# Kernel optimization log

Measured on AMD Instinct MI355X. Metric: run time of the kernel, lower is better.

## Reference

```python
import jax, jax.numpy as jnp
import numpy as np

B, EMB, H, G, F, CH, O, OC, KT = 4096, 256, 256, 8, 96, 16, 5, 10, 5
BN_EPS = 1e-3


def _grouped_linear(x, w):
    # x: [B, I], w: [G, I//G, O//G] -> [B, O]
    b = x.shape[0]
    g, ig, og = w.shape
    xg = x.reshape(b, g, ig)
    return jnp.einsum('bgi,gio->bgo', xg, w).reshape(b, g * og)


def _gru_cell(x, h, k, rk, bias):
    # keras GRUCell, reset_after=True; gate order z, r, h; bias: [2, 3H]
    xs = x @ k + bias[0]
    hs = h @ rk + bias[1]
    xz, xr, xh = jnp.split(xs, 3, axis=-1)
    hz, hr, hh = jnp.split(hs, 3, axis=-1)
    z = jax.nn.sigmoid(xz + hz)
    r = jax.nn.sigmoid(xr + hr)
    cand = jnp.tanh(xh + r * hh)
    return z * h + (1.0 - z) * cand


def setup_inputs() -> dict:
    key = jax.random.key(0)
    ks = jax.random.split(key, 20)
    w = lambda i, shape: (jax.random.normal(ks[i], shape, dtype=jnp.float32) * 0.05)
    inp = {
        'emb': jax.random.normal(ks[0], (B, EMB), dtype=jnp.float32),
        'c0': jax.random.normal(ks[1], (B, 1, F, CH), dtype=jnp.float32),
        'df_dec_state': jax.random.normal(ks[2], (B, 2 * H), dtype=jnp.float32),
        'df_convp_buf': jax.random.normal(ks[3], (B, KT - 1, F, CH), dtype=jnp.float32),
        'w_in': w(4, (G, EMB // G, H // G)),
        'gru_k0': w(5, (H, 3 * H)),
        'gru_rk0': w(6, (H, 3 * H)),
        'gru_b0': w(7, (2, 3 * H)),
        'gru_k1': w(8, (H, 3 * H)),
        'gru_rk1': w(9, (H, 3 * H)),
        'gru_b1': w(10, (2, 3 * H)),
        'w_out': w(11, (G, H // G, (F * OC) // G)),
        'fc_a_w': w(12, (H, 1)),
        'fc_a_b': jnp.zeros((1,), dtype=jnp.float32),
        'conv_w': w(13, (KT, 1, CH // 2, OC)),  # grouped conv, groups=gcd(16,10)=2
        'pw_w': w(14, (OC, OC)),                # 1x1 pointwise, no bias
        'bn_gamma': jnp.ones((OC,), dtype=jnp.float32),
        'bn_beta': jnp.zeros((OC,), dtype=jnp.float32),
        'bn_mean': jnp.zeros((OC,), dtype=jnp.float32),
        'bn_var': jnp.ones((OC,), dtype=jnp.float32),
    }
    return inp


def reference(emb, c0, df_dec_state, df_convp_buf,
              w_in, gru_k0, gru_rk0, gru_b0, gru_k1, gru_rk1, gru_b1,
              w_out, fc_a_w, fc_a_b, conv_w, pw_w,
              bn_gamma, bn_beta, bn_mean, bn_var):
    b = emb.shape[0]
    # SqueezedGRUStep: grouped linear in-proj + ReLU
    x_in = jax.nn.relu(_grouped_linear(emb, w_in))  # [B, H]
    h0 = df_dec_state[:, :H]
    h1 = df_dec_state[:, H:]
    out0 = _gru_cell(x_in, h0, gru_k0, gru_rk0, gru_b0)
    out1 = _gru_cell(out0, h1, gru_k1, gru_rk1, gru_b1)
    new_state = jnp.concatenate([out0, out1], axis=-1)  # [B, 2H]
    c = out1 + x_in  # gru_skip = identity

    # causal conv step: concat buffer + current frame -> [B, KT, F, CH]
    x = jnp.concatenate([df_convp_buf, c0], axis=1)
    new_buf = x[:, 1:, :, :]
    # grouped conv (groups=2), kernel (KT,1), valid over the KT frames -> last frame
    xg = x.reshape(b, KT, F, 2, CH // 2)                 # [B,T,F,g,i]
    wg = conv_w.reshape(KT, CH // 2, 2, OC // 2)         # [T,i,g,o]
    y = jnp.einsum('btfgi,tigo->bfgo', xg, wg).reshape(b, F, OC)
    # separable pointwise 1x1 conv
    y = y @ pw_w
    # batch norm (inference) + relu
    inv = jax.lax.rsqrt(bn_var + BN_EPS)
    y = (y - bn_mean) * inv * bn_gamma + bn_beta
    c0_out = jax.nn.relu(y)                              # [B, F, OC]

    alpha = jax.nn.sigmoid(emb @ jnp.zeros_like(fc_a_w) + c @ fc_a_w + fc_a_b)  # [B,1]
    c_out = jnp.tanh(_grouped_linear(c, w_out)).reshape(b, F, OC)
    c_out = c_out + c0_out
    # DfOutputReshapeMF: [B,1,F,O*2] -> [B,O,1,F,2]
    coefs = c_out.reshape(b, 1, F, O, 2).transpose(0, 3, 1, 2, 4)
    return (coefs, alpha, new_state, new_buf)
```

## Files before the change

kernel.cpp:

```cpp
#include <hip/hip_runtime.h>

typedef unsigned short u16;
typedef __attribute__((ext_vector_type(8))) u16 u16x8;
typedef __attribute__((ext_vector_type(8))) __bf16 bf16x8;
typedef __attribute__((ext_vector_type(4))) float f32x4;

#define ALPHA_OFF   3932160
#define NST_OFF     3936256
#define NBUF_OFF    6033408

__device__ __forceinline__ u16 f2bf(float f) {
  unsigned u = __builtin_bit_cast(unsigned, f);
  u += 0x7fffu + ((u >> 16) & 1u);
  return (u16)(u >> 16);
}
__device__ __forceinline__ float bf2f(u16 v) {
  return __builtin_bit_cast(float, (unsigned)v << 16);
}
__device__ __forceinline__ float fsig(float x) { return 1.f / (1.f + __expf(-x)); }
__device__ __forceinline__ float ftanh(float x) {
  x = fminf(15.f, fmaxf(-15.f, x));
  float e = __expf(2.f * x);
  return (e - 1.f) / (e + 1.f);
}
__device__ __forceinline__ f32x4 mfma16(u16x8 a, u16x8 b, f32x4 c) {
  return __builtin_amdgcn_mfma_f32_16x16x32_bf16(
      __builtin_bit_cast(bf16x8, a), __builtin_bit_cast(bf16x8, b), c, 0, 0, 0);
}
__device__ __forceinline__ void gload16(const void* g, void* l) {
  __builtin_amdgcn_global_load_lds(
      (const __attribute__((address_space(1))) void*)g,
      (__attribute__((address_space(3))) void*)l, 16, 0, 0);
}

__global__ __launch_bounds__(256) void wprep_kernel(
    const float* __restrict__ gk0, const float* __restrict__ grk0,
    const float* __restrict__ gk1, const float* __restrict__ grk1,
    u16* __restrict__ W2) {
  __shared__ u16 tl[64][65];
  int nb = blockIdx.x, kb = blockIdx.y, L = blockIdx.z;
  const float* src = (kb < 4) ? (L ? gk1 : gk0) : (L ? grk1 : grk0);
  int kbase = (kb & 3) * 64;
  u16* dst = W2 + (size_t)L * 768 * 512;
  int tid = threadIdx.x, c = tid & 63, r4 = tid >> 6;
  for (int rr = 0; rr < 64; rr += 4) {
    int k = kbase + rr + r4, n = nb * 64 + c;
    tl[rr + r4][c] = f2bf(src[(size_t)k * 768 + n]);
  }
  __syncthreads();
  for (int rr = 0; rr < 64; rr += 4) {
    int n = nb * 64 + rr + r4, k = kb * 64 + c;
    dst[(size_t)n * 512 + k] = tl[c][rr + r4];
  }
}

__global__ __launch_bounds__(256) void prep_kernel(
    const float* __restrict__ emb, const float* __restrict__ dec,
    const float* __restrict__ w_in, u16* __restrict__ A0, u16* __restrict__ A1) {
  __shared__ float wl[8192];
  __shared__ float el[16][256];
  int tid = threadIdx.x, rowBase = blockIdx.x * 16;
  for (int i = tid; i < 8192; i += 256) wl[i] = w_in[i];
  for (int i = tid; i < 4096; i += 256)
    el[i >> 8][i & 255] = emb[(size_t)(rowBase + (i >> 8)) * 256 + (i & 255)];
  __syncthreads();
  int g = tid >> 5, o = tid & 31;
  for (int r = 0; r < 16; ++r) {
    float acc = 0.f;
#pragma unroll
    for (int i = 0; i < 32; ++i) acc += el[r][g * 32 + i] * wl[g * 1024 + i * 32 + o];
    A0[(size_t)(rowBase + r) * 512 + tid] = f2bf(fmaxf(acc, 0.f));
  }
  for (int i = tid; i < 8192; i += 256) {
    int r = i >> 9, c = i & 511;
    u16 q = f2bf(dec[(size_t)(rowBase + r) * 512 + c]);
    if (c < 256) A0[(size_t)(rowBase + r) * 512 + 256 + c] = q;
    else         A1[(size_t)(rowBase + r) * 512 + c] = q;
  }
}

template <int LAYER>
__global__ __launch_bounds__(256) void gru_kernel(
    const u16* __restrict__ Ain,
    const u16* __restrict__ W2,
    const float* __restrict__ dec,
    const float* __restrict__ bias,
    float* __restrict__ nst,
    u16* __restrict__ a1out,
    const u16* __restrict__ xbf,
    float* __restrict__ c_f32) {
  __shared__ __align__(16) u16 lsA[2][64][32];
  __shared__ __align__(16) u16 lsB[2][3][64][32];
  int tid = threadIdx.x, lane = tid & 63, wave = tid >> 6;
  int m0 = lane & 15, quad = lane >> 4;
  int rowBase = blockIdx.x * 64, jz = blockIdx.y * 64, cw = wave * 16;
  f32x4 acc[4][4];
#pragma unroll
  for (int gi = 0; gi < 4; ++gi)
#pragma unroll
    for (int rb = 0; rb < 4; ++rb) acc[gi][rb] = (f32x4){0.f, 0.f, 0.f, 0.f};

  int rS = tid >> 2, qS = tid & 3;
  auto stage = [&](int buf, int k0) {
    gload16(Ain + (size_t)(rowBase + rS) * 512 + k0 + qS * 8, &lsA[buf][rS][qS * 8]);
#pragma unroll
    for (int g = 0; g < 3; ++g)
      gload16(W2 + (size_t)(g * 256 + jz + rS) * 512 + k0 + qS * 8,
              &lsB[buf][g][rS][qS * 8]);
  };

  stage(0, 0);
  for (int step = 0; step < 16; ++step) {
    __syncthreads();
    if (step < 15) stage((step & 1) ^ 1, (step + 1) * 32);
    int cur = step & 1;
    u16x8 av[4], bv[3];
#pragma unroll
    for (int rb = 0; rb < 4; ++rb)
      av[rb] = *(const u16x8*)&lsA[cur][rb * 16 + m0][quad * 8];
#pragma unroll
    for (int g = 0; g < 3; ++g)
      bv[g] = *(const u16x8*)&lsB[cur][g][cw + m0][quad * 8];
#pragma unroll
    for (int rb = 0; rb < 4; ++rb) {
      acc[0][rb] = mfma16(av[rb], bv[0], acc[0][rb]);
      acc[1][rb] = mfma16(av[rb], bv[1], acc[1][rb]);
    }
    if (step < 8) {
#pragma unroll
      for (int rb = 0; rb < 4; ++rb) acc[2][rb] = mfma16(av[rb], bv[2], acc[2][rb]);
    } else {
#pragma unroll
      for (int rb = 0; rb < 4; ++rb) acc[3][rb] = mfma16(av[rb], bv[2], acc[3][rb]);
    }
  }

  int col = jz + cw + m0;
  float bz = bias[col] + bias[768 + col];
  float br = bias[256 + col] + bias[1024 + col];
  float bxh = bias[512 + col];
  float bhh = bias[1280 + col];
  const int hoff = LAYER ? 256 : 0;
#pragma unroll
  for (int rb = 0; rb < 4; ++rb) {
#pragma unroll
    for (int i = 0; i < 4; ++i) {
      int row = rowBase + rb * 16 + quad * 4 + i;
      float h = dec[(size_t)row * 512 + hoff + col];
      float z = fsig(acc[0][rb][i] + bz);
      float r = fsig(acc[1][rb][i] + br);
      float cand = ftanh(acc[2][rb][i] + bxh + r * (acc[3][rb][i] + bhh));
      float o = z * h + (1.f - z) * cand;
      nst[(size_t)row * 512 + hoff + col] = o;
      if (LAYER == 0) {
        a1out[(size_t)row * 512 + col] = f2bf(o);
      } else {
        float c = o + bf2f(xbf[(size_t)row * 512 + col]);
        c_f32[(size_t)row * 256 + col] = c;
      }
    }
  }
}

__global__ __launch_bounds__(256) void wout_kernel(
    const float* __restrict__ c_f32, const float* __restrict__ w_out,
    float* __restrict__ outc) {
  __shared__ float cs[16][256];
  int tid = threadIdx.x, rowBase = blockIdx.x * 16;
  for (int i = tid; i < 4096; i += 256)
    cs[i >> 8][i & 255] = c_f32[(size_t)(rowBase + (i >> 8)) * 256 + (i & 255)];
  __syncthreads();
  for (int flat = tid; flat < 960; flat += 256) {
    int g = flat / 120, og = flat % 120;
    float acc[16];
#pragma unroll
    for (int r = 0; r < 16; ++r) acc[r] = 0.f;
    for (int i = 0; i < 32; ++i) {
      float w = w_out[(size_t)g * 3840 + i * 120 + og];
#pragma unroll
      for (int r = 0; r < 16; ++r) acc[r] += cs[r][g * 32 + i] * w;
    }
#pragma unroll
    for (int r = 0; r < 16; ++r)
      outc[(size_t)(rowBase + r) * 960 + flat] = ftanh(acc[r]);
  }
}

__global__ __launch_bounds__(256) void head_kernel(
    const float* __restrict__ convp, const float* __restrict__ c0,
    const float* __restrict__ c_f32,
    const float* __restrict__ conv_w, const float* __restrict__ pw_w,
    const float* __restrict__ bng, const float* __restrict__ bnb,
    const float* __restrict__ bnm, const float* __restrict__ bnv,
    const float* __restrict__ fca_w, const float* __restrict__ fca_b,
    float* __restrict__ outp) {
  __shared__ __align__(16) u16 xs[5 * 96 * 16];
  __shared__ float ybuf[96][10];
  __shared__ float cw[400];
  __shared__ float pw[100];
  __shared__ float bscale[10], bshift[10];
  __shared__ float ared[4];
  int tid = threadIdx.x, lane = tid & 63, wave = tid >> 6;
  int b = blockIdx.x;
  for (int i = tid; i < 400; i += 256) cw[i] = conv_w[i];
  if (tid < 100) pw[tid] = pw_w[tid];
  if (tid < 10) {
    float s = bng[tid] * rsqrtf(bnv[tid] + 1e-3f);
    bscale[tid] = s;
    bshift[tid] = bnb[tid] - bnm[tid] * s;
  }
  float4* nb4 = (float4*)(outp + NBUF_OFF);
  const float4* cp4 = (const float4*)convp;
  const float4* c04 = (const float4*)c0;

  for (int i = tid; i < 1920; i += 256) {
    int t = i / 384, p = i % 384;
    float4 v = (t < 4) ? cp4[(size_t)b * 1536 + i] : c04[(size_t)b * 384 + p];
    if (t >= 1) nb4[(size_t)b * 1536 + (size_t)(t - 1) * 384 + p] = v;
    ushort4 q;
    q.x = f2bf(v.x); q.y = f2bf(v.y); q.z = f2bf(v.z); q.w = f2bf(v.w);
    ((ushort4*)xs)[i] = q;
  }
  float ap = c_f32[(size_t)b * 256 + tid] * fca_w[tid];
#pragma unroll
  for (int off = 32; off > 0; off >>= 1) ap += __shfl_down(ap, off, 64);
  if (lane == 0) ared[wave] = ap;
  __syncthreads();
  if (tid == 0)
    outp[ALPHA_OFF + b] = fsig(ared[0] + ared[1] + ared[2] + ared[3] + fca_b[0]);
  if (tid < 192) {
    int f = tid >> 1, half = tid & 1;
    float a5[5] = {0.f, 0.f, 0.f, 0.f, 0.f};
#pragma unroll
    for (int t = 0; t < 5; ++t) {
      u16x8 xv = *(const u16x8*)&xs[t * 1536 + f * 16 + half * 8];
#pragma unroll
      for (int i = 0; i < 8; ++i) {
        float xf = bf2f(xv[i]);
#pragma unroll
        for (int j = 0; j < 5; ++j)
          a5[j] += xf * cw[t * 80 + i * 10 + half * 5 + j];
      }
    }
#pragma unroll
    for (int j = 0; j < 5; ++j) ybuf[f][half * 5 + j] = a5[j];
  }
  __syncthreads();
  float vals[4];
  int nv = 0;
  for (int u2 = tid; u2 < 480; u2 += 256) {
    int o = u2 / 96, f = u2 % 96;
#pragma unroll
    for (int q = 0; q < 2; ++q) {
      int p = o * 2 + q;
      float y2 = 0.f;
#pragma unroll
      for (int j = 0; j < 10; ++j) y2 += ybuf[f][j] * pw[j * 10 + p];
      float bnr = fmaxf(y2 * bscale[p] + bshift[p], 0.f);
      float wt = outp[(size_t)b * 960 + f * 10 + p];
      vals[nv++] = bnr + wt;
    }
  }
  __syncthreads();
  nv = 0;
  for (int u2 = tid; u2 < 480; u2 += 256) {
    int o = u2 / 96, f = u2 % 96;
    *(float2*)&outp[(size_t)b * 960 + o * 192 + f * 2] =
        make_float2(vals[nv], vals[nv + 1]);
    nv += 2;
  }
}

extern "C" void kernel_launch(void* const* d_in, const int* in_sizes, int n_in,
                              void* d_out, int out_size, void* d_ws, size_t ws_size,
                              hipStream_t stream) {
  const float* emb    = (const float*)d_in[0];
  const float* c0     = (const float*)d_in[1];
  const float* dec    = (const float*)d_in[2];
  const float* convp  = (const float*)d_in[3];
  const float* w_in   = (const float*)d_in[4];
  const float* gk0    = (const float*)d_in[5];
  const float* grk0   = (const float*)d_in[6];
  const float* gb0    = (const float*)d_in[7];
  const float* gk1    = (const float*)d_in[8];
  const float* grk1   = (const float*)d_in[9];
  const float* gb1    = (const float*)d_in[10];
  const float* w_out  = (const float*)d_in[11];
  const float* fca_w  = (const float*)d_in[12];
  const float* fca_b  = (const float*)d_in[13];
  const float* conv_w = (const float*)d_in[14];
  const float* pw_w   = (const float*)d_in[15];
  const float* bng    = (const float*)d_in[16];
  const float* bnb    = (const float*)d_in[17];
  const float* bnm    = (const float*)d_in[18];
  const float* bnv    = (const float*)d_in[19];
  float* out = (float*)d_out;
  char* ws = (char*)d_ws;
  u16*   A0    = (u16*)(ws + 0);
  u16*   A1    = (u16*)(ws + 4194304);
  float* c_f32 = (float*)(ws + 8388608);
  u16*   W2    = (u16*)(ws + 12582912);

  wprep_kernel<<<dim3(12, 8, 2), 256, 0, stream>>>(gk0, grk0, gk1, grk1, W2);
  prep_kernel<<<dim3(256), 256, 0, stream>>>(emb, dec, w_in, A0, A1);
  gru_kernel<0><<<dim3(64, 4), 256, 0, stream>>>(A0, W2, dec, gb0,
                                                 out + NST_OFF, A1, nullptr, nullptr);
  gru_kernel<1><<<dim3(64, 4), 256, 0, stream>>>(A1, W2 + 768 * 512, dec, gb1,
                                                 out + NST_OFF, nullptr, A0, c_f32);
  wout_kernel<<<dim3(256), 256, 0, stream>>>(c_f32, w_out, out);
  head_kernel<<<dim3(4096), 256, 0, stream>>>(convp, c0, c_f32, conv_w, pw_w,
                                              bng, bnb, bnm, bnv, fca_w, fca_b, out);
}
```

Before: 357.3 us.

## Use MFMA for grouped output projection, shrink GRU tiles, restructure prep and head kernels

Moves the grouped w_out projection from scalar FP32 FMAs to bf16 MFMA, using a new prep kernel that packs w_out into a padded bf16 layout. The GRU tile height is halved to launch twice as many blocks, and c is stored as bf16 instead of FP32. The prep kernel now handles 4 rows per block with register-held weights and vectorized loads. The head kernel is reworked to keep conv inputs in registers at 192 threads. Storing c in bf16 lowers the precision of both the alpha and output-projection paths.

New measurement: 313.9 us. 1.14x faster.

```diff
diff --git a/kernel.cpp b/kernel.cpp
--- a/kernel.cpp
+++ b/kernel.cpp
@@ -54,28 +54,48 @@
   }
 }
 
+__global__ __launch_bounds__(256) void w3prep_kernel(
+    const float* __restrict__ w_out, u16* __restrict__ W3) {
+  int g = blockIdx.x, tid = threadIdx.x;
+  for (int i = tid; i < 4096; i += 256) {
+    int col = i >> 5, k = i & 31;
+    float v = (col < 120) ? w_out[(size_t)g * 3840 + k * 120 + col] : 0.f;
+    W3[(size_t)g * 4096 + i] = f2bf(v);
+  }
+}
+
 __global__ __launch_bounds__(256) void prep_kernel(
     const float* __restrict__ emb, const float* __restrict__ dec,
     const float* __restrict__ w_in, u16* __restrict__ A0, u16* __restrict__ A1) {
-  __shared__ float wl[8192];
-  __shared__ float el[16][256];
-  int tid = threadIdx.x, rowBase = blockIdx.x * 16;
-  for (int i = tid; i < 8192; i += 256) wl[i] = w_in[i];
-  for (int i = tid; i < 4096; i += 256)
-    el[i >> 8][i & 255] = emb[(size_t)(rowBase + (i >> 8)) * 256 + (i & 255)];
-  __syncthreads();
+  __shared__ float el[4][256];
+  int tid = threadIdx.x, rowBase = blockIdx.x * 4;
+  {
+    int r = tid >> 6, c4 = tid & 63;
+    *(float4*)&el[r][c4 * 4] = ((const float4*)emb)[(size_t)(rowBase + r) * 64 + c4];
+  }
   int g = tid >> 5, o = tid & 31;
-  for (int r = 0; r < 16; ++r) {
+  float wr[32];
+#pragma unroll
+  for (int i = 0; i < 32; ++i) wr[i] = w_in[g * 1024 + i * 32 + o];
+  __syncthreads();
+#pragma unroll
+  for (int r = 0; r < 4; ++r) {
     float acc = 0.f;
 #pragma unroll
-    for (int i = 0; i < 32; ++i) acc += el[r][g * 32 + i] * wl[g * 1024 + i * 32 + o];
+    for (int i = 0; i < 32; ++i) acc += el[r][g * 32 + i] * wr[i];
     A0[(size_t)(rowBase + r) * 512 + tid] = f2bf(fmaxf(acc, 0.f));
   }
-  for (int i = tid; i < 8192; i += 256) {
-    int r = i >> 9, c = i & 511;
-    u16 q = f2bf(dec[(size_t)(rowBase + r) * 512 + c]);
-    if (c < 256) A0[(size_t)(rowBase + r) * 512 + 256 + c] = q;
-    else         A1[(size_t)(rowBase + r) * 512 + c] = q;
+  const float4* d4 = (const float4*)dec;
+#pragma unroll
+  for (int j = 0; j < 2; ++j) {
+    int idx = tid + j * 256;
+    int r = idx >> 7, c4 = idx & 127;
+    float4 v = d4[(size_t)(rowBase + r) * 128 + c4];
+    ushort4 q;
+    q.x = f2bf(v.x); q.y = f2bf(v.y); q.z = f2bf(v.z); q.w = f2bf(v.w);
+    u16* dst = (c4 < 64) ? A0 + (size_t)(rowBase + r) * 512 + 256 + c4 * 4
+                         : A1 + (size_t)(rowBase + r) * 512 + 256 + (c4 - 64) * 4;
+    *(ushort4*)dst = q;
   }
 }
 
@@ -88,21 +108,23 @@
     float* __restrict__ nst,
     u16* __restrict__ a1out,
     const u16* __restrict__ xbf,
-    float* __restrict__ c_f32) {
-  __shared__ __align__(16) u16 lsA[2][64][32];
+    u16* __restrict__ c_bf) {
+  __shared__ __align__(16) u16 lsA[2][32][32];
   __shared__ __align__(16) u16 lsB[2][3][64][32];
   int tid = threadIdx.x, lane = tid & 63, wave = tid >> 6;
   int m0 = lane & 15, quad = lane >> 4;
-  int rowBase = blockIdx.x * 64, jz = blockIdx.y * 64, cw = wave * 16;
-  f32x4 acc[4][4];
+  int rowBase = blockIdx.x * 32, jz = blockIdx.y * 64, cw = wave * 16;
+  f32x4 acc[4][2];
 #pragma unroll
   for (int gi = 0; gi < 4; ++gi)
 #pragma unroll
-    for (int rb = 0; rb < 4; ++rb) acc[gi][rb] = (f32x4){0.f, 0.f, 0.f, 0.f};
+    for (int rb = 0; rb < 2; ++rb) acc[gi][rb] = (f32x4){0.f, 0.f, 0.f, 0.f};
 
   int rS = tid >> 2, qS = tid & 3;
   auto stage = [&](int buf, int k0) {
-    gload16(Ain + (size_t)(rowBase + rS) * 512 + k0 + qS * 8, &lsA[buf][rS][qS * 8]);
+    if (tid < 128)
+      gload16(Ain + (size_t)(rowBase + rS) * 512 + k0 + qS * 8,
+              &lsA[buf][rS][qS * 8]);
 #pragma unroll
     for (int g = 0; g < 3; ++g)
       gload16(W2 + (size_t)(g * 256 + jz + rS) * 512 + k0 + qS * 8,
@@ -114,24 +136,24 @@
     __syncthreads();
     if (step < 15) stage((step & 1) ^ 1, (step + 1) * 32);
     int cur = step & 1;
-    u16x8 av[4], bv[3];
-#pragma unroll
-    for (int rb = 0; rb < 4; ++rb)
+    u16x8 av[2], bv[3];
+#pragma unroll
+    for (int rb = 0; rb < 2; ++rb)
       av[rb] = *(const u16x8*)&lsA[cur][rb * 16 + m0][quad * 8];
 #pragma unroll
     for (int g = 0; g < 3; ++g)
       bv[g] = *(const u16x8*)&lsB[cur][g][cw + m0][quad * 8];
 #pragma unroll
-    for (int rb = 0; rb < 4; ++rb) {
+    for (int rb = 0; rb < 2; ++rb) {
       acc[0][rb] = mfma16(av[rb], bv[0], acc[0][rb]);
       acc[1][rb] = mfma16(av[rb], bv[1], acc[1][rb]);
     }
     if (step < 8) {
 #pragma unroll
-      for (int rb = 0; rb < 4; ++rb) acc[2][rb] = mfma16(av[rb], bv[2], acc[2][rb]);
+      for (int rb = 0; rb < 2; ++rb) acc[2][rb] = mfma16(av[rb], bv[2], acc[2][rb]);
     } else {
 #pragma unroll
-      for (int rb = 0; rb < 4; ++rb) acc[3][rb] = mfma16(av[rb], bv[2], acc[3][rb]);
+      for (int rb = 0; rb < 2; ++rb) acc[3][rb] = mfma16(av[rb], bv[2], acc[3][rb]);
     }
   }
 
@@ -142,7 +164,7 @@
   float bhh = bias[1280 + col];
   const int hoff = LAYER ? 256 : 0;
 #pragma unroll
-  for (int rb = 0; rb < 4; ++rb) {
+  for (int rb = 0; rb < 2; ++rb) {
 #pragma unroll
     for (int i = 0; i < 4; ++i) {
       int row = rowBase + rb * 16 + quad * 4 + i;
@@ -156,118 +178,145 @@
         a1out[(size_t)row * 512 + col] = f2bf(o);
       } else {
         float c = o + bf2f(xbf[(size_t)row * 512 + col]);
-        c_f32[(size_t)row * 256 + col] = c;
+        c_bf[(size_t)row * 256 + col] = f2bf(c);
       }
     }
   }
 }
 
 __global__ __launch_bounds__(256) void wout_kernel(
-    const float* __restrict__ c_f32, const float* __restrict__ w_out,
+    const u16* __restrict__ c_bf, const u16* __restrict__ W3,
     float* __restrict__ outc) {
-  __shared__ float cs[16][256];
-  int tid = threadIdx.x, rowBase = blockIdx.x * 16;
-  for (int i = tid; i < 4096; i += 256)
-    cs[i >> 8][i & 255] = c_f32[(size_t)(rowBase + (i >> 8)) * 256 + (i & 255)];
-  __syncthreads();
-  for (int flat = tid; flat < 960; flat += 256) {
-    int g = flat / 120, og = flat % 120;
-    float acc[16];
-#pragma unroll
-    for (int r = 0; r < 16; ++r) acc[r] = 0.f;
-    for (int i = 0; i < 32; ++i) {
-      float w = w_out[(size_t)g * 3840 + i * 120 + og];
-#pragma unroll
-      for (int r = 0; r < 16; ++r) acc[r] += cs[r][g * 32 + i] * w;
-    }
-#pragma unroll
-    for (int r = 0; r < 16; ++r)
-      outc[(size_t)(rowBase + r) * 960 + flat] = ftanh(acc[r]);
-  }
-}
-
-__global__ __launch_bounds__(256) void head_kernel(
+  __shared__ __align__(16) u16 lsA[64][32];
+  __shared__ __align__(16) u16 lsB[128][32];
+  int tid = threadIdx.x, lane = tid & 63, wave = tid >> 6;
+  int m0 = lane & 15, quad = lane >> 4;
+  int rowBase = blockIdx.x * 64, g = blockIdx.y;
+  {
+    int r = tid >> 2, q = tid & 3;
+    gload16(c_bf + (size_t)(rowBase + r) * 256 + g * 32 + q * 8, &lsA[r][q * 8]);
+    gload16(W3 + (size_t)g * 4096 + (size_t)r * 32 + q * 8, &lsB[r][q * 8]);
+    gload16(W3 + (size_t)g * 4096 + (size_t)(64 + r) * 32 + q * 8, &lsB[64 + r][q * 8]);
+  }
+  __syncthreads();
+  int cw = wave * 32;
+  f32x4 acc[4][2];
+#pragma unroll
+  for (int rb = 0; rb < 4; ++rb)
+#pragma unroll
+    for (int cb = 0; cb < 2; ++cb) acc[rb][cb] = (f32x4){0.f, 0.f, 0.f, 0.f};
+  u16x8 bv[2];
+#pragma unroll
+  for (int cb = 0; cb < 2; ++cb)
+    bv[cb] = *(const u16x8*)&lsB[cw + cb * 16 + m0][quad * 8];
+#pragma unroll
+  for (int rb = 0; rb < 4; ++rb) {
+    u16x8 av = *(const u16x8*)&lsA[rb * 16 + m0][quad * 8];
+#pragma unroll
+    for (int cb = 0; cb < 2; ++cb) acc[rb][cb] = mfma16(av, bv[cb], acc[rb][cb]);
+  }
+#pragma unroll
+  for (int cb = 0; cb < 2; ++cb) {
+    int cg = cw + cb * 16 + m0;
+    if (cg < 120) {
+#pragma unroll
+      for (int rb = 0; rb < 4; ++rb)
+#pragma unroll
+        for (int i = 0; i < 4; ++i)
+          outc[(size_t)(rowBase + rb * 16 + quad * 4 + i) * 960 + g * 120 + cg] =
+              ftanh(acc[rb][cb][i]);
+    }
+  }
+}
+
+__global__ __launch_bounds__(192) void head_kernel(
     const float* __restrict__ convp, const float* __restrict__ c0,
-    const float* __restrict__ c_f32,
+    const u16* __restrict__ c_bf,
     const float* __restrict__ conv_w, const float* __restrict__ pw_w,
     const float* __restrict__ bng, const float* __restrict__ bnb,
     const float* __restrict__ bnm, const float* __restrict__ bnv,
     const float* __restrict__ fca_w, const float* __restrict__ fca_b,
     float* __restrict__ outp) {
-  __shared__ __align__(16) u16 xs[5 * 96 * 16];
-  __shared__ float ybuf[96][10];
   __shared__ float cw[400];
-  __shared__ float pw[100];
-  __shared__ float bscale[10], bshift[10];
-  __shared__ float ared[4];
+  __shared__ float pws[100];
+  __shared__ float bsc[10], bsh[10];
+  __shared__ float ybuf[96][11];
+  __shared__ float ared[3];
   int tid = threadIdx.x, lane = tid & 63, wave = tid >> 6;
   int b = blockIdx.x;
-  for (int i = tid; i < 400; i += 256) cw[i] = conv_w[i];
-  if (tid < 100) pw[tid] = pw_w[tid];
+  int f = tid >> 1, half = tid & 1;
+  const float4* cp4 = (const float4*)convp;
+  const float4* c04 = (const float4*)c0;
+  float4* nb4 = (float4*)(outp + NBUF_OFF);
+
+  float4 xa[5], xb[5];
+#pragma unroll
+  for (int t = 0; t < 4; ++t) {
+    size_t idx = (size_t)b * 1536 + t * 384 + f * 4 + half * 2;
+    xa[t] = cp4[idx]; xb[t] = cp4[idx + 1];
+  }
+  {
+    size_t idx = (size_t)b * 384 + f * 4 + half * 2;
+    xa[4] = c04[idx]; xb[4] = c04[idx + 1];
+  }
+  float tmp[5];
+#pragma unroll
+  for (int k = 0; k < 5; ++k) {
+    int u = tid + k * 192;
+    tmp[k] = outp[(size_t)b * 960 + (u % 96) * 10 + (u / 96)];
+  }
+  float ap = bf2f(c_bf[(size_t)b * 256 + tid]) * fca_w[tid];
+  if (tid < 64) ap += bf2f(c_bf[(size_t)b * 256 + 192 + tid]) * fca_w[192 + tid];
+
+  for (int i = tid; i < 400; i += 192) cw[i] = conv_w[i];
+  if (tid < 100) pws[tid] = pw_w[tid];
   if (tid < 10) {
     float s = bng[tid] * rsqrtf(bnv[tid] + 1e-3f);
-    bscale[tid] = s;
-    bshift[tid] = bnb[tid] - bnm[tid] * s;
-  }
-  float4* nb4 = (float4*)(outp + NBUF_OFF);
-  const float4* cp4 = (const float4*)convp;
-  const float4* c04 = (const float4*)c0;
-
-  for (int i = tid; i < 1920; i += 256) {
-    int t = i / 384, p = i % 384;
-    float4 v = (t < 4) ? cp4[(size_t)b * 1536 + i] : c04[(size_t)b * 384 + p];
-    if (t >= 1) nb4[(size_t)b * 1536 + (size_t)(t - 1) * 384 + p] = v;
-    ushort4 q;
-    q.x = f2bf(v.x); q.y = f2bf(v.y); q.z = f2bf(v.z); q.w = f2bf(v.w);
-    ((ushort4*)xs)[i] = q;
-  }
-  float ap = c_f32[(size_t)b * 256 + tid] * fca_w[tid];
+    bsc[tid] = s;
+    bsh[tid] = bnb[tid] - bnm[tid] * s;
+  }
+#pragma unroll
+  for (int t = 1; t < 5; ++t) {
+    size_t idx = (size_t)b * 1536 + (t - 1) * 384 + f * 4 + half * 2;
+    nb4[idx] = xa[t]; nb4[idx + 1] = xb[t];
+  }
 #pragma unroll
   for (int off = 32; off > 0; off >>= 1) ap += __shfl_down(ap, off, 64);
   if (lane == 0) ared[wave] = ap;
   __syncthreads();
+  float a5[5] = {0.f, 0.f, 0.f, 0.f, 0.f};
+#pragma unroll
+  for (int t = 0; t < 5; ++t) {
+    const float* xr0 = (const float*)&xa[t];
+    const float* xr1 = (const float*)&xb[t];
+#pragma unroll
+    for (int i = 0; i < 8; ++i) {
+      float xf = (i < 4) ? xr0[i] : xr1[i - 4];
+#pragma unroll
+      for (int j = 0; j < 5; ++j)
+        a5[j] += xf * cw[t * 80 + i * 10 + half * 5 + j];
+    }
+  }
+#pragma unroll
+  for (int j = 0; j < 5; ++j) ybuf[f][half * 5 + j] = a5[j];
+  __syncthreads();
   if (tid == 0)
-    outp[ALPHA_OFF + b] = fsig(ared[0] + ared[1] + ared[2] + ared[3] + fca_b[0]);
-  if (tid < 192) {
-    int f = tid >> 1, half = tid & 1;
-    float a5[5] = {0.f, 0.f, 0.f, 0.f, 0.f};
-#pragma unroll
-    for (int t = 0; t < 5; ++t) {
-      u16x8 xv = *(const u16x8*)&xs[t * 1536 + f * 16 + half * 8];
-#pragma unroll
-      for (int i = 0; i < 8; ++i) {
-        float xf = bf2f(xv[i]);
-#pragma unroll
-        for (int j = 0; j < 5; ++j)
-          a5[j] += xf * cw[t * 80 + i * 10 + half * 5 + j];
-      }
-    }
-#pragma unroll
-    for (int j = 0; j < 5; ++j) ybuf[f][half * 5 + j] = a5[j];
-  }
-  __syncthreads();
-  float vals[4];
-  int nv = 0;
-  for (int u2 = tid; u2 < 480; u2 += 256) {
-    int o = u2 / 96, f = u2 % 96;
-#pragma unroll
-    for (int q = 0; q < 2; ++q) {
-      int p = o * 2 + q;
-      float y2 = 0.f;
-#pragma unroll
-      for (int j = 0; j < 10; ++j) y2 += ybuf[f][j] * pw[j * 10 + p];
-      float bnr = fmaxf(y2 * bscale[p] + bshift[p], 0.f);
-      float wt = outp[(size_t)b * 960 + f * 10 + p];
-      vals[nv++] = bnr + wt;
-    }
-  }
-  __syncthreads();
-  nv = 0;
-  for (int u2 = tid; u2 < 480; u2 += 256) {
-    int o = u2 / 96, f = u2 % 96;
-    *(float2*)&outp[(size_t)b * 960 + o * 192 + f * 2] =
-        make_float2(vals[nv], vals[nv + 1]);
-    nv += 2;
+    outp[ALPHA_OFF + b] = fsig(ared[0] + ared[1] + ared[2] + fca_b[0]);
+  float vals[5];
+#pragma unroll
+  for (int k = 0; k < 5; ++k) {
+    int u = tid + k * 192;
+    int p = u / 96, ff = u % 96;
+    float y2 = 0.f;
+#pragma unroll
+    for (int j = 0; j < 10; ++j) y2 += ybuf[ff][j] * pws[j * 10 + p];
+    vals[k] = fmaxf(y2 * bsc[p] + bsh[p], 0.f) + tmp[k];
+  }
+#pragma unroll
+  for (int k = 0; k < 5; ++k) {
+    int u = tid + k * 192;
+    int p = u / 96, ff = u % 96;
+    outp[(size_t)b * 960 + (p >> 1) * 192 + ff * 2 + (p & 1)] = vals[k];
   }
 }
 
@@ -296,18 +345,20 @@
   const float* bnv    = (const float*)d_in[19];
   float* out = (float*)d_out;
   char* ws = (char*)d_ws;
-  u16*   A0    = (u16*)(ws + 0);
-  u16*   A1    = (u16*)(ws + 4194304);
-  float* c_f32 = (float*)(ws + 8388608);
-  u16*   W2    = (u16*)(ws + 12582912);
+  u16* A0   = (u16*)(ws + 0);
+  u16* A1   = (u16*)(ws + 4194304);
+  u16* c_bf = (u16*)(ws + 8388608);
+  u16* W2   = (u16*)(ws + 10485760);
+  u16* W3   = (u16*)(ws + 12058624);
 
   wprep_kernel<<<dim3(12, 8, 2), 256, 0, stream>>>(gk0, grk0, gk1, grk1, W2);
-  prep_kernel<<<dim3(256), 256, 0, stream>>>(emb, dec, w_in, A0, A1);
-  gru_kernel<0><<<dim3(64, 4), 256, 0, stream>>>(A0, W2, dec, gb0,
-                                                 out + NST_OFF, A1, nullptr, nullptr);
-  gru_kernel<1><<<dim3(64, 4), 256, 0, stream>>>(A1, W2 + 768 * 512, dec, gb1,
-                                                 out + NST_OFF, nullptr, A0, c_f32);
-  wout_kernel<<<dim3(256), 256, 0, stream>>>(c_f32, w_out, out);
-  head_kernel<<<dim3(4096), 256, 0, stream>>>(convp, c0, c_f32, conv_w, pw_w,
+  w3prep_kernel<<<dim3(8), 256, 0, stream>>>(w_out, W3);
+  prep_kernel<<<dim3(1024), 256, 0, stream>>>(emb, dec, w_in, A0, A1);
+  gru_kernel<0><<<dim3(128, 4), 256, 0, stream>>>(A0, W2, dec, gb0,
+                                                  out + NST_OFF, A1, nullptr, nullptr);
+  gru_kernel<1><<<dim3(128, 4), 256, 0, stream>>>(A1, W2 + 768 * 512, dec, gb1,
+                                                  out + NST_OFF, nullptr, A0, c_bf);
+  wout_kernel<<<dim3(64, 8), 256, 0, stream>>>(c_bf, W3, out);
+  head_kernel<<<dim3(4096), 192, 0, stream>>>(convp, c0, c_bf, conv_w, pw_w,
                                               bng, bnb, bnm, bnv, fca_w, fca_b, out);
 }
```
